# Optimization experiments

Measured on AMD Instinct MI355X. Metric: run time of the kernel, lower is better.

Reference implementation:

```python
import jax, jax.numpy as jnp
import numpy as np

B, N, C = 4, 4096, 64
K1, K2 = 4, 6
MLP1 = [128, 64, 64]
MLP2 = [128, 64]
EPS = 1e-5


def _sqdist(a, b):
    # a: [B,N,3], b: [B,M,3] -> [B,N,M]
    return (jnp.sum(a * a, -1)[:, :, None] + jnp.sum(b * b, -1)[:, None, :]
            - 2.0 * jnp.einsum('bnc,bmc->bnm', a, b))


def _knn_idx(k, xyz, new_xyz):
    # matches knn_point: topk of -square_distance(new_xyz, xyz)
    _, idx = jax.lax.top_k(-_sqdist(new_xyz, xyz), k)
    return idx  # [B,S,k]


def _gather(points, idx):
    # index_points: points [B,N,C], idx [B,S,K] -> [B,S,K,C]
    return jax.vmap(lambda p, i: p[i])(points, idx)


def _conv_bn_relu(x, w, g, b):
    # 1x1 Conv2d (no bias) + BatchNorm2d (train mode) + ReLU, channels-last
    y = jnp.einsum('bnkc,oc->bnko', x, w)
    m = jnp.mean(y, axis=(0, 1, 2), keepdims=True)
    v = jnp.var(y, axis=(0, 1, 2), keepdims=True)
    return jax.nn.relu((y - m) * jax.lax.rsqrt(v + EPS) * g + b)


def _quat_mul(a, b):
    # Hamilton product, matches mul_q_point ordering
    aw, ax, ay, az = a[..., 0], a[..., 1], a[..., 2], a[..., 3]
    bw, bx, by, bz = b[..., 0], b[..., 1], b[..., 2], b[..., 3]
    return jnp.stack([
        aw * bw - ax * bx - ay * by - az * bz,
        aw * bx + ax * bw + ay * bz - az * by,
        aw * by - ax * bz + ay * bw + az * bx,
        aw * bz + ax * by - ay * bx + az * bw], axis=-1)


def _inv_q(q):
    n2 = jnp.sum(q * q, -1, keepdims=True) + 1e-10
    return jnp.concatenate([q[..., :1], -q[..., 1:]], -1) / n2


def _qrot(q, v):
    # rotate points v [B,M,3] by quaternion q [B,4] via q * (0,v) * q^-1
    vq = jnp.concatenate([jnp.zeros(v.shape[:-1] + (1,), v.dtype), v], -1)
    qb = q[:, None, :]
    return _quat_mul(_quat_mul(qb, vq), _inv_q(q)[:, None, :])[..., 1:]


def setup_inputs() -> dict:
    key = jax.random.key(0)
    ks = jax.random.split(key, 32)

    def rn(i, shape, s=1.0):
        return jax.random.normal(ks[i], shape, jnp.float32) * s

    inp = {
        'pos1': rn(0, (B, N, 3)),
        'pos2': rn(1, (B, N, 3)),
        'feat1': rn(2, (B, N, C)),
        'feat2': rn(3, (B, N, C)),
        'q_coarse': rn(4, (B, 4)),
        't_coarse': rn(5, (B, 3)),
    }
    c1 = [2 * C + 3] + MLP1
    for i in range(len(MLP1)):
        inp['w1_%d' % i] = rn(6 + i, (c1[i + 1], c1[i]), 0.1)
        inp['g1_%d' % i] = jnp.ones((c1[i + 1],), jnp.float32)
        inp['b1_%d' % i] = jnp.zeros((c1[i + 1],), jnp.float32)
    c2 = [MLP1[-1] + C + 3] + MLP2
    for i in range(len(MLP2)):
        inp['w2_%d' % i] = rn(12 + i, (c2[i + 1], c2[i]), 0.1)
        inp['g2_%d' % i] = jnp.ones((c2[i + 1],), jnp.float32)
        inp['b2_%d' % i] = jnp.zeros((c2[i + 1],), jnp.float32)
    inp['wq'] = rn(20, (4, MLP2[-1]), 0.01)
    inp['bq'] = jnp.zeros((4,), jnp.float32)
    inp['wt'] = rn(21, (3, MLP2[-1]), 0.01)
    inp['bt'] = jnp.zeros((3,), jnp.float32)
    return inp


def reference(pos1, pos2, feat1, feat2, q_coarse, t_coarse,
              w1_0, g1_0, b1_0, w1_1, g1_1, b1_1, w1_2, g1_2, b1_2,
              w2_0, g2_0, b2_0, w2_1, g2_1, b2_1, wq, bq, wt, bt):
    # warp pos1 by the coarse pose (q, t)
    pos1_w = _qrot(q_coarse, pos1) + t_coarse[:, None, :]

    # cross-cloud KNN grouping (FlowEmbedding first stage)
    idx2 = _knn_idx(K2, pos2, pos1_w)                      # [B,N,K2]
    xd2 = _gather(pos2, idx2) - pos1_w[:, :, None, :]      # [B,N,K2,3]
    f2g = _gather(feat2, idx2)                             # [B,N,K2,C]
    f1r = jnp.broadcast_to(feat1[:, :, None, :], (B, N, K2, C))
    x = jnp.concatenate([xd2, f2g, f1r], -1)               # [B,N,K2,131]
    for w, g, b in ((w1_0, g1_0, b1_0), (w1_1, g1_1, b1_1), (w1_2, g1_2, b1_2)):
        x = _conv_bn_relu(x, w, g, b)
    fe = jnp.sum(x, axis=2)                                # [B,N,64] sum pool over neighbors

    # self KNN grouping (FlowEmbedding second stage)
    idx1 = _knn_idx(K1, pos1_w, pos1_w)                    # [B,N,K1]
    xd1 = _gather(pos1_w, idx1) - pos1_w[:, :, None, :]
    feg = _gather(fe, idx1)
    f1r2 = jnp.broadcast_to(feat1[:, :, None, :], (B, N, K1, C))
    x = jnp.concatenate([xd1, feg, f1r2], -1)              # [B,N,K1,131]
    for w, g, b in ((w2_0, g2_0, b2_0), (w2_1, g2_1, b2_1)):
        x = _conv_bn_relu(x, w, g, b)
    pooled = jnp.sum(jnp.sum(x, axis=2), axis=1)           # [B,64] sum pool

    # pose delta heads + quaternion composition
    q_det = pooled @ wq.T + bq
    q_det = q_det / (jnp.linalg.norm(q_det, axis=-1, keepdims=True) + 1e-10)
    t_det = pooled @ wt.T + bt
    q_new = _quat_mul(q_det, q_coarse)
    q_new = q_new / (jnp.linalg.norm(q_new, axis=-1, keepdims=True) + 1e-10)
    t_new = _qrot(q_det, t_coarse[:, None, :])[:, 0, :] + t_det
    return jnp.concatenate([q_new, t_new], -1)             # [B,7]
```

## Files before the change

### kernel.cpp

```cpp
#include <hip/hip_runtime.h>
#include <math.h>

#define B_ 4
#define N_ 4096
#define C_ 64
#define K1_ 4
#define K2_ 6
#define EPS_ 1e-5f
#define BN_ (B_ * N_)
#define NCH_ 8
#define CHP_ 512
#define STKD_ 16

typedef __attribute__((ext_vector_type(8))) short bf16x8;
typedef __attribute__((ext_vector_type(4))) float f32x4;
typedef __attribute__((ext_vector_type(2))) float f32x2;

__device__ __forceinline__ unsigned short f2bf(float f) {
  unsigned int u = __float_as_uint(f);
  unsigned int r = (u + 0x7fffu + ((u >> 16) & 1u)) >> 16;
  return (unsigned short)r;
}
__device__ __forceinline__ float bf2f(unsigned short u) {
  return __uint_as_float(((unsigned int)u) << 16);
}
__device__ __forceinline__ void unpack8(uint4 u, float* f) {
  unsigned* up = (unsigned*)&u;
#pragma unroll
  for (int w = 0; w < 4; ++w) {
    f[2 * w] = __uint_as_float(up[w] << 16);
    f[2 * w + 1] = __uint_as_float(up[w] & 0xFFFF0000u);
  }
}

template <int K>
__device__ __forceinline__ void insKi(int* kd, int k) {
  int x = k;
#pragma unroll
  for (int u = 0; u < K; ++u) {
    int lo = min(kd[u], x);
    x = max(kd[u], x);
    kd[u] = lo;
  }
}

__global__ __launch_bounds__(256) void k_init(
    const float* __restrict__ w1_0, const float* __restrict__ w1_1,
    const float* __restrict__ w1_2, const float* __restrict__ w2_0,
    const float* __restrict__ w2_1, unsigned short* __restrict__ Wf2a,
    unsigned short* __restrict__ Wf1a, unsigned short* __restrict__ Wfe,
    unsigned short* __restrict__ Wf1b, unsigned short* __restrict__ wb1,
    unsigned short* __restrict__ wb2, unsigned short* __restrict__ wb4,
    const float* __restrict__ pos1, const float* __restrict__ pos2,
    const float* __restrict__ qc, const float* __restrict__ tc,
    float4* __restrict__ pts4w, float4* __restrict__ pts4p,
    float4* __restrict__ pairW, float4* __restrict__ pairP,
    float* __restrict__ zbase) {
  int t = blockIdx.x * 256 + threadIdx.x;
  int m = blockIdx.y;
  if (m < 7) {
    switch (m) {
      case 0:
        if (t < 8192) Wf2a[t] = f2bf(w1_0[(t >> 6) * 131 + 3 + (t & 63)]);
        break;
      case 1:
        if (t < 8192) Wf1a[t] = f2bf(w1_0[(t >> 6) * 131 + 67 + (t & 63)]);
        break;
      case 2:
        if (t < 8192) Wfe[t] = f2bf(w2_0[(t >> 6) * 131 + 3 + (t & 63)]);
        break;
      case 3:
        if (t < 8192) Wf1b[t] = f2bf(w2_0[(t >> 6) * 131 + 67 + (t & 63)]);
        break;
      case 4:
        if (t < 8192) wb1[t] = f2bf(w1_1[t]);
        break;
      case 5:
        if (t < 4096) wb2[t] = f2bf(w1_2[t]);
        break;
      default:
        if (t < 8192) wb4[t] = f2bf(w2_1[t]);
        break;
    }
    return;
  }
  if (m == 8) {
    if (t < 10240) zbase[t] = 0.f;
    return;
  }
  if (t >= BN_) return;
  int b = t / N_;
  float qw = qc[b * 4 + 0], qx = qc[b * 4 + 1], qy = qc[b * 4 + 2], qz = qc[b * 4 + 3];
  float vx = pos1[t * 3 + 0], vy = pos1[t * 3 + 1], vz = pos1[t * 3 + 2];
  float aw = -(qx * vx + qy * vy + qz * vz);
  float ax = qw * vx + qy * vz - qz * vy;
  float ay = qw * vy - qx * vz + qz * vx;
  float az = qw * vz + qx * vy - qy * vx;
  float n2 = qw * qw + qx * qx + qy * qy + qz * qz + 1e-10f;
  float bw = qw / n2, bx = -qx / n2, by = -qy / n2, bz = -qz / n2;
  float rx = aw * bx + ax * bw + ay * bz - az * by;
  float ry = aw * by - ax * bz + ay * bw + az * bx;
  float rz = aw * bz + ax * by - ay * bx + az * bw;
  rx += tc[b * 3 + 0];
  ry += tc[b * 3 + 1];
  rz += tc[b * 3 + 2];
  float rw2 = rx * rx + ry * ry + rz * rz;
  pts4w[t] = make_float4(rx, ry, rz, rw2);
  int p = t >> 1, h = t & 1;
  float* bwp = (float*)&pairW[(size_t)2 * p];
  bwp[0 + h] = rx; bwp[2 + h] = ry; bwp[4 + h] = rz; bwp[6 + h] = rw2;
  float px = pos2[t * 3 + 0], py = pos2[t * 3 + 1], pz = pos2[t * 3 + 2];
  float pw2 = px * px + py * py + pz * pz;
  pts4p[t] = make_float4(px, py, pz, pw2);
  float* bpp = (float*)&pairP[(size_t)2 * p];
  bpp[0 + h] = px; bpp[2 + h] = py; bpp[4 + h] = pz; bpp[6 + h] = pw2;
}

__device__ __forceinline__ void proj_mfma_tail(const unsigned short* Xs, int tid,
                                               int row0,
                                               const unsigned short* __restrict__ Wb,
                                               unsigned short* __restrict__ dst) {
  constexpr int SP = 72;
  int l = tid & 63, wv = tid >> 6;
  int lm = l & 15, quad = l >> 4;
  int n0 = wv * 32;
  f32x4 acc[4][2];
#pragma unroll
  for (int rt = 0; rt < 4; ++rt)
#pragma unroll
    for (int ct = 0; ct < 2; ++ct) acc[rt][ct] = (f32x4)(0.f);
#pragma unroll
  for (int k0 = 0; k0 < 64; k0 += 32) {
    bf16x8 a[4], b[2];
#pragma unroll
    for (int rt = 0; rt < 4; ++rt)
      a[rt] = *(const bf16x8*)&Xs[(rt * 16 + lm) * SP + k0 + quad * 8];
#pragma unroll
    for (int ct = 0; ct < 2; ++ct)
      b[ct] = *(const bf16x8*)&Wb[(size_t)(n0 + ct * 16 + lm) * 64 + k0 + quad * 8];
#pragma unroll
    for (int rt = 0; rt < 4; ++rt)
#pragma unroll
      for (int ct = 0; ct < 2; ++ct)
        acc[rt][ct] =
            __builtin_amdgcn_mfma_f32_16x16x32_bf16(a[rt], b[ct], acc[rt][ct], 0, 0, 0);
  }
#pragma unroll
  for (int rt = 0; rt < 4; ++rt)
#pragma unroll
    for (int ct = 0; ct < 2; ++ct)
#pragma unroll
      for (int r = 0; r < 4; ++r) {
        int row = row0 + rt * 16 + quad * 4 + r;
        dst[(size_t)row * 128 + n0 + ct * 16 + lm] = f2bf(acc[rt][ct][r]);
      }
}

template <int K>
__device__ __forceinline__ void knn_chunk(const f32x4* __restrict__ PT, int base,
                                          float4 qv, int tid, int (*st)[256],
                                          int* __restrict__ orow) {
  f32x2 qq2 = (f32x2)(qv.w);
  f32x2 m2x = (f32x2)(-2.f * qv.x);
  f32x2 m2y = (f32x2)(-2.f * qv.y);
  f32x2 m2z = (f32x2)(-2.f * qv.z);
  int kd[K];
#pragma unroll
  for (int t = 0; t < K; ++t) kd[t] = 0x7fffffff;
  int kbd = 0x7fffffff;
  int ptr = 0;
  for (int jj = 0; jj < CHP_; jj += 8) {
    f32x2 d[4];
#pragma unroll
    for (int gq = 0; gq < 2; ++gq) {
      f32x4 e0 = PT[jj + gq * 4 + 0];
      f32x4 e1 = PT[jj + gq * 4 + 1];
      f32x4 e2 = PT[jj + gq * 4 + 2];
      f32x4 e3 = PT[jj + gq * 4 + 3];
      d[gq * 2 + 0] = __builtin_elementwise_fma(
          m2x, e0.xy,
          __builtin_elementwise_fma(m2y, e0.zw,
                                    __builtin_elementwise_fma(m2z, e1.xy, e1.zw + qq2)));
      d[gq * 2 + 1] = __builtin_elementwise_fma(
          m2x, e2.xy,
          __builtin_elementwise_fma(m2y, e2.zw,
                                    __builtin_elementwise_fma(m2z, e3.xy, e3.zw + qq2)));
    }
    int j0 = base + jj;
#pragma unroll
    for (int p = 0; p < 4; ++p) {
      int ka = (int)((__float_as_uint(d[p].x) & 0xFFFFF000u) | (unsigned)(j0 + 2 * p));
      int kb = (int)((__float_as_uint(d[p].y) & 0xFFFFF000u) | (unsigned)(j0 + 2 * p + 1));
      st[ptr][tid] = ka;
      ptr += (ka < kbd) ? 1 : 0;
      st[ptr][tid] = kb;
      ptr += (kb < kbd) ? 1 : 0;
    }
    if (__ballot(ptr >= STKD_ - 8)) {
      for (int i = 0; i < ptr; ++i) insKi<K>(kd, st[i][tid]);
      ptr = 0;
      kbd = kd[K - 1];
    }
  }
  for (int i = 0; i < ptr; ++i) insKi<K>(kd, st[i][tid]);
#pragma unroll
  for (int t = 0; t < K; ++t) orow[t] = kd[t];
}

__global__ __launch_bounds__(256) void k_knnproj(
    const float4* __restrict__ pts4w, const float4* __restrict__ pairW,
    const float4* __restrict__ pairP, int* __restrict__ outK,
    const float* __restrict__ feat2, const unsigned short* __restrict__ Wf2a,
    unsigned short* __restrict__ P2a, const float* __restrict__ feat1,
    const unsigned short* __restrict__ Wf1a, unsigned short* __restrict__ P1a,
    const unsigned short* __restrict__ Wf1b, unsigned short* __restrict__ P1b) {
  __shared__ int st[STKD_][256];
  int tid = threadIdx.x;
  int bid = blockIdx.x;
  if (bid < 768) {
    const float* src;
    const unsigned short* Wb;
    unsigned short* dst;
    switch (bid >> 8) {
      case 0: src = feat2; Wb = Wf2a; dst = P2a; break;
      case 1: src = feat1; Wb = Wf1a; dst = P1a; break;
      default: src = feat1; Wb = Wf1b; dst = P1b; break;
    }
    unsigned short* Xs = (unsigned short*)&st[0][0];
    int row0 = (bid & 255) * 64;
    for (int e = tid; e < 64 * 16; e += 256) {
      int r = e >> 4, s = e & 15;
      float4 v = *(const float4*)&src[(size_t)(row0 + r) * 64 + s * 4];
      ushort4 o;
      o.x = f2bf(v.x); o.y = f2bf(v.y); o.z = f2bf(v.z); o.w = f2bf(v.w);
      *(ushort4*)&Xs[r * 72 + s * 4] = o;
    }
    __syncthreads();
    proj_mfma_tail(Xs, tid, row0, Wb, dst);
    return;
  }
  int kbid = bid - 768;
  int x = kbid & 15, y = (kbid >> 4) & 7, z = kbid >> 7;
  int b = z & 3;
  int which = z >> 2;
  const f32x4* __restrict__ PT =
      (const f32x4*)((which ? pairW : pairP) + (size_t)b * N_ + y * CHP_);
  int base = y * CHP_;
  int n = x * 256 + tid;
  float4 qv = pts4w[(size_t)b * N_ + n];
  int* orow = &outK[((size_t)which * BN_ * NCH_ + (size_t)(b * N_ + n) * NCH_ + y) * 6];
  if (which == 0)
    knn_chunk<6>(PT, base, qv, tid, st, orow);
  else
    knn_chunk<4>(PT, base, qv, tid, st, orow);
}

__global__ __launch_bounds__(256) void k_feproj(const unsigned short* __restrict__ y3,
                                                const float* __restrict__ stat,
                                                const float* __restrict__ g,
                                                const float* __restrict__ bb,
                                                const unsigned short* __restrict__ Wfe,
                                                unsigned short* __restrict__ Pfe) {
  constexpr int SP = 72;
  __shared__ unsigned short Xs[64 * SP];
  __shared__ float scl[C_], shf[C_];
  int tid = threadIdx.x;
  if (tid < C_) {
    int c = tid;
    float s = 0.f, s2 = 0.f;
#pragma unroll
    for (int u = 0; u < 8; ++u) {
      s += stat[c * 8 + u];
      s2 += stat[C_ * 8 + c * 8 + u];
    }
    const float invM = 1.f / (float)(BN_ * K2_);
    float m = s * invM;
    float v = s2 * invM - m * m;
    float sc = g[c] * rsqrtf(v + EPS_);
    scl[c] = sc;
    shf[c] = bb[c] - m * sc;
  }
  __syncthreads();
  int row0 = blockIdx.x * 64;
  for (int e = tid; e < 64 * 16; e += 256) {
    int r = e >> 4, s = e & 15;
    size_t base = ((size_t)(row0 + r) * K2_) * C_ + s * 4;
    float a0 = 0.f, a1 = 0.f, a2 = 0.f, a3 = 0.f;
#pragma unroll
    for (int k = 0; k < K2_; ++k) {
      ushort4 u = *(const ushort4*)&y3[base + (size_t)k * C_];
      a0 += fmaxf(fmaf(bf2f(u.x), scl[s * 4 + 0], shf[s * 4 + 0]), 0.f);
      a1 += fmaxf(fmaf(bf2f(u.y), scl[s * 4 + 1], shf[s * 4 + 1]), 0.f);
      a2 += fmaxf(fmaf(bf2f(u.z), scl[s * 4 + 2], shf[s * 4 + 2]), 0.f);
      a3 += fmaxf(fmaf(bf2f(u.w), scl[s * 4 + 3], shf[s * 4 + 3]), 0.f);
    }
    ushort4 o;
    o.x = f2bf(a0); o.y = f2bf(a1); o.z = f2bf(a2); o.w = f2bf(a3);
    *(ushort4*)&Xs[r * SP + s * 4] = o;
  }
  __syncthreads();
  proj_mfma_tail(Xs, tid, row0, Wfe, Pfe);
}

template <int KNN>
__global__ __launch_bounds__(256) void k_asm(
    const float* __restrict__ Wfull,
    const float4* __restrict__ nbrPts, const float4* __restrict__ qryPts,
    const unsigned short* __restrict__ Pj, const unsigned short* __restrict__ Pn,
    const int* __restrict__ outK,
    unsigned short* __restrict__ yout, float* __restrict__ statOut) {
  __shared__ float Wx[3][128];
  __shared__ float red[16][128];
  __shared__ int idxL[33][6];
  int tid = threadIdx.x;
  int row0 = blockIdx.x * 128;
  int first = row0 / KNN;
  int nq = (row0 + 127) / KNN - first + 1;
  if (tid < 128) {
    Wx[0][tid] = Wfull[tid * 131 + 0];
    Wx[1][tid] = Wfull[tid * 131 + 1];
    Wx[2][tid] = Wfull[tid * 131 + 2];
  }
  if (tid < nq) {
    int q = first + tid;
    int km[6];
#pragma unroll
    for (int u = 0; u < 6; ++u) km[u] = 0x7fffffff;
    size_t ib = (size_t)q * (NCH_ * 6);
    if (KNN == 6) {
      for (int c = 0; c < NCH_ * 6; ++c) insKi<6>(km, outK[ib + c]);
    } else {
      for (int ch = 0; ch < NCH_; ++ch)
#pragma unroll
        for (int u = 0; u < 4; ++u) insKi<4>(km, outK[ib + ch * 6 + u]);
    }
#pragma unroll
    for (int u = 0; u < KNN; ++u) idxL[tid][u] = km[u] & 0xFFF;
  }
  __syncthreads();
  int cg = tid & 15, rg = tid >> 4;
  int c0 = cg * 8;
  float wx0[8], wx1[8], wx2[8];
#pragma unroll
  for (int u = 0; u < 8; ++u) {
    wx0[u] = Wx[0][c0 + u];
    wx1[u] = Wx[1][c0 + u];
    wx2[u] = Wx[2][c0 + u];
  }
  float s1[8], s2[8];
#pragma unroll
  for (int u = 0; u < 8; ++u) { s1[u] = 0.f; s2[u] = 0.f; }
#pragma unroll
  for (int i = 0; i < 8; ++i) {
    int row = row0 + rg * 8 + i;
    int g = row / KNN;
    int j = idxL[g - first][row - g * KNN];
    int gj = ((g >> 12) << 12) + j;
    float4 pw = qryPts[g];
    float4 pn4 = nbrPts[gj];
    float xd0 = pn4.x - pw.x;
    float xd1 = pn4.y - pw.y;
    float xd2 = pn4.z - pw.z;
    uint4 uj = *(const uint4*)&Pj[(size_t)gj * 128 + c0];
    uint4 un = *(const uint4*)&Pn[(size_t)g * 128 + c0];
    float yj[8], yn[8];
    unpack8(uj, yj);
    unpack8(un, yn);
    ushort4 o0, o1;
    unsigned short ob[8];
#pragma unroll
    for (int u = 0; u < 8; ++u) {
      float v = yj[u] + yn[u];
      v = fmaf(xd0, wx0[u], v);
      v = fmaf(xd1, wx1[u], v);
      v = fmaf(xd2, wx2[u], v);
      s1[u] += v;
      s2[u] = fmaf(v, v, s2[u]);
      ob[u] = f2bf(v);
    }
    o0.x = ob[0]; o0.y = ob[1]; o0.z = ob[2]; o0.w = ob[3];
    o1.x = ob[4]; o1.y = ob[5]; o1.z = ob[6]; o1.w = ob[7];
    *(ushort4*)&yout[(size_t)row * 128 + c0] = o0;
    *(ushort4*)&yout[(size_t)row * 128 + c0 + 4] = o1;
  }
  int slot = blockIdx.x & 7;
#pragma unroll
  for (int u = 0; u < 8; ++u) red[rg][c0 + u] = s1[u];
  __syncthreads();
  if (tid < 128) {
    float s = 0.f;
#pragma unroll
    for (int r = 0; r < 16; ++r) s += red[r][tid];
    atomicAdd(&statOut[tid * 8 + slot], s);
  }
  __syncthreads();
#pragma unroll
  for (int u = 0; u < 8; ++u) red[rg][c0 + u] = s2[u];
  __syncthreads();
  if (tid < 128) {
    float s = 0.f;
#pragma unroll
    for (int r = 0; r < 16; ++r) s += red[r][tid];
    atomicAdd(&statOut[128 * 8 + tid * 8 + slot], s);
  }
}

template <int CIN, int COUT, int KP>
__global__ __launch_bounds__(256) void k_layer_mfma(
    const unsigned short* __restrict__ Wb,
    const unsigned short* __restrict__ yprev,
    const float* __restrict__ statPrev, const float* __restrict__ gPrev,
    const float* __restrict__ bPrev, float prevInvM,
    unsigned short* __restrict__ yout,
    float* __restrict__ statOut) {
  constexpr int SP = KP + 8;
  constexpr int CST = COUT + 8;
  constexpr int CT = COUT / 64;
  __shared__ unsigned short Xs[64 * SP];
  __shared__ float scl[CIN];
  __shared__ float shf[CIN];

  int tid = threadIdx.x;
  int row0 = blockIdx.x * 64;

  for (int c = tid; c < CIN; c += 256) {
    float s = 0.f, s2 = 0.f;
#pragma unroll
    for (int u = 0; u < 8; ++u) {
      s += statPrev[c * 8 + u];
      s2 += statPrev[CIN * 8 + c * 8 + u];
    }
    float m = s * prevInvM;
    float v = s2 * prevInvM - m * m;
    float sc = gPrev[c] * rsqrtf(v + EPS_);
    scl[c] = sc;
    shf[c] = bPrev[c] - m * sc;
  }
  __syncthreads();
  constexpr int S8 = KP / 8;
  for (int e = tid; e < 64 * S8; e += 256) {
    int r = e / S8, s = e - r * S8;
    int row = row0 + r;
    uint4 u = *(const uint4*)&yprev[(size_t)row * CIN + s * 8];
    uint4 o;
    unsigned* up = (unsigned*)&u;
    unsigned* op = (unsigned*)&o;
#pragma unroll
    for (int w = 0; w < 4; ++w) {
      int c = s * 8 + w * 2;
      float lo = __uint_as_float(up[w] << 16);
      float hi = __uint_as_float(up[w] & 0xFFFF0000u);
      float rl = fmaxf(fmaf(lo, scl[c], shf[c]), 0.f);
      float rh = fmaxf(fmaf(hi, scl[c + 1], shf[c + 1]), 0.f);
      op[w] = (unsigned)f2bf(rl) | ((unsigned)f2bf(rh) << 16);
    }
    *(uint4*)&Xs[r * SP + s * 8] = o;
  }
  __syncthreads();

  int l = tid & 63, wv = tid >> 6;
  int lm = l & 15, quad = l >> 4;
  int n0 = wv * (COUT / 4);

  f32x4 acc[4][CT];
#pragma unroll
  for (int rt = 0; rt < 4; ++rt)
#pragma unroll
    for (int ct = 0; ct < CT; ++ct) acc[rt][ct] = (f32x4)(0.f);

#pragma unroll
  for (int k0 = 0; k0 < KP; k0 += 32) {
    bf16x8 a[4], b[CT];
#pragma unroll
    for (int rt = 0; rt < 4; ++rt)
      a[rt] = *(const bf16x8*)&Xs[(rt * 16 + lm) * SP + k0 + quad * 8];
#pragma unroll
    for (int ct = 0; ct < CT; ++ct)
      b[ct] = *(const bf16x8*)&Wb[(size_t)(n0 + ct * 16 + lm) * KP + k0 + quad * 8];
#pragma unroll
    for (int rt = 0; rt < 4; ++rt)
#pragma unroll
      for (int ct = 0; ct < CT; ++ct)
        acc[rt][ct] =
            __builtin_amdgcn_mfma_f32_16x16x32_bf16(a[rt], b[ct], acc[rt][ct], 0, 0, 0);
  }

  int slot = blockIdx.x & 7;
#pragma unroll
  for (int ct = 0; ct < CT; ++ct) {
    float s1 = 0.f, s2 = 0.f;
#pragma unroll
    for (int rt = 0; rt < 4; ++rt)
#pragma unroll
      for (int r = 0; r < 4; ++r) {
        float v = acc[rt][ct][r];
        s1 += v;
        s2 += v * v;
      }
    s1 += __shfl_xor(s1, 16);
    s1 += __shfl_xor(s1, 32);
    s2 += __shfl_xor(s2, 16);
    s2 += __shfl_xor(s2, 32);
    if (quad == 0) {
      int col = n0 + ct * 16 + lm;
      atomicAdd(&statOut[col * 8 + slot], s1);
      atomicAdd(&statOut[COUT * 8 + col * 8 + slot], s2);
    }
  }

  __syncthreads();
  unsigned short* Ys = Xs;
#pragma unroll
  for (int rt = 0; rt < 4; ++rt)
#pragma unroll
    for (int ct = 0; ct < CT; ++ct)
#pragma unroll
      for (int r = 0; r < 4; ++r)
        Ys[(rt * 16 + quad * 4 + r) * CST + n0 + ct * 16 + lm] = f2bf(acc[rt][ct][r]);
  __syncthreads();
  constexpr int SO = COUT / 8;
  for (int e = tid; e < 64 * SO; e += 256) {
    int r = e / SO, c0 = (e - r * SO) * 8;
    uint4 v = *(const uint4*)&Ys[r * CST + c0];
    *(uint4*)&yout[((size_t)(row0 + r)) * COUT + c0] = v;
  }
}

__global__ __launch_bounds__(256) void k_pooled(const unsigned short* __restrict__ y5,
                                                const float* __restrict__ stat,
                                                const float* __restrict__ g,
                                                const float* __restrict__ bb,
                                                float* __restrict__ pooled) {
  __shared__ float scl[C_], shf[C_];
  __shared__ float red[16][C_];
  if (threadIdx.x < C_) {
    int c = threadIdx.x;
    float s = 0.f, s2 = 0.f;
#pragma unroll
    for (int u = 0; u < 8; ++u) {
      s += stat[c * 8 + u];
      s2 += stat[C_ * 8 + c * 8 + u];
    }
    const float invM = 1.f / (float)(BN_ * K1_);
    float m = s * invM;
    float v = s2 * invM - m * m;
    float sc = g[c] * rsqrtf(v + EPS_);
    scl[c] = sc;
    shf[c] = bb[c] - m * sc;
  }
  __syncthreads();
  int cq = threadIdx.x & 15, rr = threadIdx.x >> 4;
  int c0 = cq * 4;
  int row0 = blockIdx.x * 64;
  int b = blockIdx.x >> 8;
  float a0 = 0.f, a1 = 0.f, a2 = 0.f, a3 = 0.f;
#pragma unroll
  for (int i = 0; i < 4; ++i) {
    int row = row0 + rr * 4 + i;
    ushort4 u = *(const ushort4*)&y5[(size_t)row * C_ + c0];
    a0 += fmaxf(fmaf(bf2f(u.x), scl[c0 + 0], shf[c0 + 0]), 0.f);
    a1 += fmaxf(fmaf(bf2f(u.y), scl[c0 + 1], shf[c0 + 1]), 0.f);
    a2 += fmaxf(fmaf(bf2f(u.z), scl[c0 + 2], shf[c0 + 2]), 0.f);
    a3 += fmaxf(fmaf(bf2f(u.w), scl[c0 + 3], shf[c0 + 3]), 0.f);
  }
  red[rr][c0 + 0] = a0;
  red[rr][c0 + 1] = a1;
  red[rr][c0 + 2] = a2;
  red[rr][c0 + 3] = a3;
  __syncthreads();
  if (threadIdx.x < C_) {
    float s = 0.f;
#pragma unroll
    for (int r = 0; r < 16; ++r) s += red[r][threadIdx.x];
    atomicAdd(&pooled[(b * C_ + threadIdx.x) * 8 + (blockIdx.x & 7)], s);
  }
}

__global__ void k_final(const float* __restrict__ pooled, const float* __restrict__ wq,
                        const float* __restrict__ bq, const float* __restrict__ wt,
                        const float* __restrict__ bt, const float* __restrict__ qc,
                        const float* __restrict__ tc, float* __restrict__ out) {
  int b = threadIdx.x;
  if (b >= B_) return;
  float P[C_];
#pragma unroll
  for (int c = 0; c < C_; ++c) {
    float s = 0.f;
#pragma unroll
    for (int u = 0; u < 8; ++u) s += pooled[(b * C_ + c) * 8 + u];
    P[c] = s;
  }
  float qd[4];
#pragma unroll
  for (int i = 0; i < 4; ++i) {
    float s = bq[i];
#pragma unroll
    for (int c = 0; c < C_; ++c) s = fmaf(P[c], wq[i * C_ + c], s);
    qd[i] = s;
  }
  float td[3];
#pragma unroll
  for (int i = 0; i < 3; ++i) {
    float s = bt[i];
#pragma unroll
    for (int c = 0; c < C_; ++c) s = fmaf(P[c], wt[i * C_ + c], s);
    td[i] = s;
  }
  float nq = sqrtf(qd[0] * qd[0] + qd[1] * qd[1] + qd[2] * qd[2] + qd[3] * qd[3]) + 1e-10f;
#pragma unroll
  for (int i = 0; i < 4; ++i) qd[i] /= nq;
  float cw = qc[b * 4 + 0], cx = qc[b * 4 + 1], cyy = qc[b * 4 + 2], cz = qc[b * 4 + 3];
  float qnw = qd[0] * cw - qd[1] * cx - qd[2] * cyy - qd[3] * cz;
  float qnx = qd[0] * cx + qd[1] * cw + qd[2] * cz - qd[3] * cyy;
  float qny = qd[0] * cyy - qd[1] * cz + qd[2] * cw + qd[3] * cx;
  float qnz = qd[0] * cz + qd[1] * cyy - qd[2] * cx + qd[3] * cw;
  float nn = sqrtf(qnw * qnw + qnx * qnx + qny * qny + qnz * qnz) + 1e-10f;
  float vx = tc[b * 3 + 0], vy = tc[b * 3 + 1], vz = tc[b * 3 + 2];
  float aw = -(qd[1] * vx + qd[2] * vy + qd[3] * vz);
  float ax = qd[0] * vx + qd[2] * vz - qd[3] * vy;
  float ay = qd[0] * vy - qd[1] * vz + qd[3] * vx;
  float az = qd[0] * vz + qd[1] * vy - qd[2] * vx;
  float n2 = qd[0] * qd[0] + qd[1] * qd[1] + qd[2] * qd[2] + qd[3] * qd[3] + 1e-10f;
  float bw = qd[0] / n2, bx = -qd[1] / n2, by = -qd[2] / n2, bz = -qd[3] / n2;
  float rx = aw * bx + ax * bw + ay * bz - az * by;
  float ry = aw * by - ax * bz + ay * bw + az * bx;
  float rz = aw * bz + ax * by - ay * bx + az * bw;
  out[b * 7 + 0] = qnw / nn;
  out[b * 7 + 1] = qnx / nn;
  out[b * 7 + 2] = qny / nn;
  out[b * 7 + 3] = qnz / nn;
  out[b * 7 + 4] = rx + td[0];
  out[b * 7 + 5] = ry + td[1];
  out[b * 7 + 6] = rz + td[2];
}

extern "C" void kernel_launch(void* const* d_in, const int* in_sizes, int n_in,
                              void* d_out, int out_size, void* d_ws, size_t ws_size,
                              hipStream_t stream) {
  const float* pos1 = (const float*)d_in[0];
  const float* pos2 = (const float*)d_in[1];
  const float* feat1 = (const float*)d_in[2];
  const float* feat2 = (const float*)d_in[3];
  const float* qc = (const float*)d_in[4];
  const float* tc = (const float*)d_in[5];
  const float* w1_0 = (const float*)d_in[6];
  const float* g1_0 = (const float*)d_in[7];
  const float* b1_0 = (const float*)d_in[8];
  const float* w1_1 = (const float*)d_in[9];
  const float* g1_1 = (const float*)d_in[10];
  const float* b1_1 = (const float*)d_in[11];
  const float* w1_2 = (const float*)d_in[12];
  const float* g1_2 = (const float*)d_in[13];
  const float* b1_2 = (const float*)d_in[14];
  const float* w2_0 = (const float*)d_in[15];
  const float* g2_0 = (const float*)d_in[16];
  const float* b2_0 = (const float*)d_in[17];
  const float* w2_1 = (const float*)d_in[18];
  const float* g2_1 = (const float*)d_in[19];
  const float* b2_1 = (const float*)d_in[20];
  const float* wq = (const float*)d_in[21];
  const float* bq = (const float*)d_in[22];
  const float* wt = (const float*)d_in[23];
  const float* bt = (const float*)d_in[24];

  float* ws = (float*)d_ws;
  const size_t off_stat = 0;
  const size_t off_pool = 8192;
  const size_t off_wb = 10240;
  const size_t off_pts4w = 36864;
  const size_t off_pts4p = 102400;
  const size_t off_pairW = 167936;
  const size_t off_pairP = 233472;
  const size_t off_knnK = 299008;
  const size_t off_P2a = 1871872;
  const size_t off_P1a = 2920448;
  const size_t off_P1b = 3969024;
  const size_t off_Pfe = 5017600;
  const size_t off_yA = 6066176;
  const size_t off_yB = 12357632;

  float* stat0 = ws + off_stat;
  float* stat1 = stat0 + 2048;
  float* stat2 = stat1 + 1024;
  float* stat3 = stat2 + 1024;
  float* stat4 = stat3 + 2048;
  float* pooled = ws + off_pool;
  unsigned short* Wf2a = (unsigned short*)(ws + off_wb);
  unsigned short* Wf1a = Wf2a + 8192;
  unsigned short* Wfe = Wf1a + 8192;
  unsigned short* Wf1b = Wfe + 8192;
  unsigned short* wb1 = Wf1b + 8192;
  unsigned short* wb2 = wb1 + 8192;
  unsigned short* wb4 = wb2 + 4096;
  float4* pts4w = (float4*)(ws + off_pts4w);
  float4* pts4p = (float4*)(ws + off_pts4p);
  float4* pairW = (float4*)(ws + off_pairW);
  float4* pairP = (float4*)(ws + off_pairP);
  int* knnK = (int*)(ws + off_knnK);
  unsigned short* P2a = (unsigned short*)(ws + off_P2a);
  unsigned short* P1a = (unsigned short*)(ws + off_P1a);
  unsigned short* P1b = (unsigned short*)(ws + off_P1b);
  unsigned short* Pfe = (unsigned short*)(ws + off_Pfe);
  unsigned short* yA = (unsigned short*)(ws + off_yA);
  unsigned short* yB = (unsigned short*)(ws + off_yB);

  k_init<<<dim3(64, 9), 256, 0, stream>>>(w1_0, w1_1, w1_2, w2_0, w2_1, Wf2a, Wf1a,
                                          Wfe, Wf1b, wb1, wb2, wb4, pos1, pos2, qc, tc,
                                          pts4w, pts4p, pairW, pairP, ws + off_stat);

  k_knnproj<<<dim3(768 + 1024), 256, 0, stream>>>(pts4w, pairW, pairP, knnK, feat2,
                                                  Wf2a, P2a, feat1, Wf1a, P1a, Wf1b,
                                                  P1b);

  k_asm<K2_><<<dim3(98304 / 128), 256, 0, stream>>>(w1_0, pts4p, pts4w, P2a, P1a, knnK,
                                                    yA, stat0);
  k_layer_mfma<128, 64, 128><<<dim3(1536), 256, 0, stream>>>(
      wb1, yA, stat0, g1_0, b1_0, 1.f / 98304.f, yB, stat1);
  k_layer_mfma<64, 64, 64><<<dim3(1536), 256, 0, stream>>>(
      wb2, yB, stat1, g1_1, b1_1, 1.f / 98304.f, yA, stat2);
  k_feproj<<<dim3(256), 256, 0, stream>>>(yA, stat2, g1_2, b1_2, Wfe, Pfe);
  k_asm<K1_><<<dim3(65536 / 128), 256, 0, stream>>>(
      w2_0, pts4w, pts4w, Pfe, P1b, knnK + (size_t)BN_ * NCH_ * 6, yA, stat3);
  k_layer_mfma<128, 64, 128><<<dim3(1024), 256, 0, stream>>>(
      wb4, yA, stat3, g2_0, b2_0, 1.f / 65536.f, yB, stat4);
  k_pooled<<<dim3(65536 / 64), 256, 0, stream>>>(yB, stat4, g2_1, b2_1, pooled);
  k_final<<<dim3(1), 64, 0, stream>>>(pooled, wq, bq, wt, bt, qc, tc, (float*)d_out);
}
```

Measured before the change: 358.8 us.

## Recompute gathered first-layer activations instead of materializing 128-channel intermediate

The assembly kernel now only computes batch-norm statistics and writes the resolved neighbor indices, no longer storing the 128-channel bf16 pre-activation tensor. The next layer kernel re-gathers the projected features and positions by index, recomputes the pre-activation, applies BN+ReLU and feeds the MFMA directly. This removes a large write and read of the intermediate tensor at the cost of doing the gather and arithmetic twice. The layer kernels are also specialised to a fixed 64-column output.

```diff
diff --git a/kernel.cpp b/kernel.cpp
--- a/kernel.cpp
+++ b/kernel.cpp
@@ -303,12 +303,11 @@
 }
 
 template <int KNN>
-__global__ __launch_bounds__(256) void k_asm(
-    const float* __restrict__ Wfull,
-    const float4* __restrict__ nbrPts, const float4* __restrict__ qryPts,
-    const unsigned short* __restrict__ Pj, const unsigned short* __restrict__ Pn,
-    const int* __restrict__ outK,
-    unsigned short* __restrict__ yout, float* __restrict__ statOut) {
+__global__ __launch_bounds__(256) void k_stat0(
+    const float* __restrict__ Wfull, const float4* __restrict__ nbrPts,
+    const float4* __restrict__ qryPts, const unsigned short* __restrict__ Pj,
+    const unsigned short* __restrict__ Pn, const int* __restrict__ outK,
+    int* __restrict__ idxM, float* __restrict__ statOut) {
   __shared__ float Wx[3][128];
   __shared__ float red[16][128];
   __shared__ int idxL[33][6];
@@ -334,8 +333,13 @@
 #pragma unroll
         for (int u = 0; u < 4; ++u) insKi<4>(km, outK[ib + ch * 6 + u]);
     }
-#pragma unroll
-    for (int u = 0; u < KNN; ++u) idxL[tid][u] = km[u] & 0xFFF;
+    int bb = (q >> 12) << 12;
+#pragma unroll
+    for (int u = 0; u < KNN; ++u) {
+      int gj = bb + (km[u] & 0xFFF);
+      idxL[tid][u] = gj;
+      idxM[(size_t)q * KNN + u] = gj;
+    }
   }
   __syncthreads();
   int cg = tid & 15, rg = tid >> 4;
@@ -354,8 +358,7 @@
   for (int i = 0; i < 8; ++i) {
     int row = row0 + rg * 8 + i;
     int g = row / KNN;
-    int j = idxL[g - first][row - g * KNN];
-    int gj = ((g >> 12) << 12) + j;
+    int gj = idxL[g - first][row - g * KNN];
     float4 pw = qryPts[g];
     float4 pn4 = nbrPts[gj];
     float xd0 = pn4.x - pw.x;
@@ -366,8 +369,6 @@
     float yj[8], yn[8];
     unpack8(uj, yj);
     unpack8(un, yn);
-    ushort4 o0, o1;
-    unsigned short ob[8];
 #pragma unroll
     for (int u = 0; u < 8; ++u) {
       float v = yj[u] + yn[u];
@@ -376,12 +377,7 @@
       v = fmaf(xd2, wx2[u], v);
       s1[u] += v;
       s2[u] = fmaf(v, v, s2[u]);
-      ob[u] = f2bf(v);
-    }
-    o0.x = ob[0]; o0.y = ob[1]; o0.z = ob[2]; o0.w = ob[3];
-    o1.x = ob[4]; o1.y = ob[5]; o1.z = ob[6]; o1.w = ob[7];
-    *(ushort4*)&yout[(size_t)row * 128 + c0] = o0;
-    *(ushort4*)&yout[(size_t)row * 128 + c0 + 4] = o1;
+    }
   }
   int slot = blockIdx.x & 7;
 #pragma unroll
@@ -405,30 +401,35 @@
   }
 }
 
-template <int CIN, int COUT, int KP>
-__global__ __launch_bounds__(256) void k_layer_mfma(
+template <int KNN>
+__global__ __launch_bounds__(256) void k_layerG(
     const unsigned short* __restrict__ Wb,
-    const unsigned short* __restrict__ yprev,
+    const float* __restrict__ Wfull, const float4* __restrict__ nbrPts,
+    const float4* __restrict__ qryPts, const unsigned short* __restrict__ Pj,
+    const unsigned short* __restrict__ Pn, const int* __restrict__ idxM,
     const float* __restrict__ statPrev, const float* __restrict__ gPrev,
     const float* __restrict__ bPrev, float prevInvM,
     unsigned short* __restrict__ yout,
     float* __restrict__ statOut) {
+  constexpr int KP = 128, COUT = 64;
   constexpr int SP = KP + 8;
   constexpr int CST = COUT + 8;
-  constexpr int CT = COUT / 64;
   __shared__ unsigned short Xs[64 * SP];
-  __shared__ float scl[CIN];
-  __shared__ float shf[CIN];
+  __shared__ float scl[KP];
+  __shared__ float shf[KP];
+  __shared__ float Wx[3][128];
+  __shared__ int gjL[64];
+  __shared__ float xdL[3][64];
 
   int tid = threadIdx.x;
   int row0 = blockIdx.x * 64;
 
-  for (int c = tid; c < CIN; c += 256) {
+  for (int c = tid; c < KP; c += 256) {
     float s = 0.f, s2 = 0.f;
 #pragma unroll
     for (int u = 0; u < 8; ++u) {
       s += statPrev[c * 8 + u];
-      s2 += statPrev[CIN * 8 + c * 8 + u];
+      s2 += statPrev[KP * 8 + c * 8 + u];
     }
     float m = s * prevInvM;
     float v = s2 * prevInvM - m * m;
@@ -436,64 +437,78 @@
     scl[c] = sc;
     shf[c] = bPrev[c] - m * sc;
   }
-  __syncthreads();
-  constexpr int S8 = KP / 8;
-  for (int e = tid; e < 64 * S8; e += 256) {
-    int r = e / S8, s = e - r * S8;
+  if (tid < 128) {
+    Wx[0][tid] = Wfull[tid * 131 + 0];
+    Wx[1][tid] = Wfull[tid * 131 + 1];
+    Wx[2][tid] = Wfull[tid * 131 + 2];
+  }
+  if (tid < 64) {
+    int row = row0 + tid;
+    int g = row / KNN;
+    int gj = idxM[(size_t)g * KNN + (row - g * KNN)];
+    gjL[tid] = gj;
+    float4 pw = qryPts[g];
+    float4 pn4 = nbrPts[gj];
+    xdL[0][tid] = pn4.x - pw.x;
+    xdL[1][tid] = pn4.y - pw.y;
+    xdL[2][tid] = pn4.z - pw.z;
+  }
+  __syncthreads();
+  for (int e = tid; e < 64 * 16; e += 256) {
+    int r = e >> 4, s = e & 15;
+    int c0 = s * 8;
     int row = row0 + r;
-    uint4 u = *(const uint4*)&yprev[(size_t)row * CIN + s * 8];
-    uint4 o;
-    unsigned* up = (unsigned*)&u;
-    unsigned* op = (unsigned*)&o;
-#pragma unroll
-    for (int w = 0; w < 4; ++w) {
-      int c = s * 8 + w * 2;
-      float lo = __uint_as_float(up[w] << 16);
-      float hi = __uint_as_float(up[w] & 0xFFFF0000u);
-      float rl = fmaxf(fmaf(lo, scl[c], shf[c]), 0.f);
-      float rh = fmaxf(fmaf(hi, scl[c + 1], shf[c + 1]), 0.f);
-      op[w] = (unsigned)f2bf(rl) | ((unsigned)f2bf(rh) << 16);
-    }
-    *(uint4*)&Xs[r * SP + s * 8] = o;
+    int g = row / KNN;
+    uint4 uj = *(const uint4*)&Pj[(size_t)gjL[r] * 128 + c0];
+    uint4 un = *(const uint4*)&Pn[(size_t)g * 128 + c0];
+    float yj[8], yn[8];
+    unpack8(uj, yj);
+    unpack8(un, yn);
+    float xd0 = xdL[0][r], xd1 = xdL[1][r], xd2 = xdL[2][r];
+    unsigned short ob[8];
+#pragma unroll
+    for (int u = 0; u < 8; ++u) {
+      int c = c0 + u;
+      float v = yj[u] + yn[u];
+      v = fmaf(xd0, Wx[0][c], v);
+      v = fmaf(xd1, Wx[1][c], v);
+      v = fmaf(xd2, Wx[2][c], v);
+      ob[u] = f2bf(fmaxf(fmaf(v, scl[c], shf[c]), 0.f));
+    }
+    ushort4 o0, o1;
+    o0.x = ob[0]; o0.y = ob[1]; o0.z = ob[2]; o0.w = ob[3];
+    o1.x = ob[4]; o1.y = ob[5]; o1.z = ob[6]; o1.w = ob[7];
+    *(ushort4*)&Xs[r * SP + c0] = o0;
+    *(ushort4*)&Xs[r * SP + c0 + 4] = o1;
   }
   __syncthreads();
 
   int l = tid & 63, wv = tid >> 6;
   int lm = l & 15, quad = l >> 4;
-  int n0 = wv * (COUT / 4);
-
-  f32x4 acc[4][CT];
-#pragma unroll
-  for (int rt = 0; rt < 4; ++rt)
-#pragma unroll
-    for (int ct = 0; ct < CT; ++ct) acc[rt][ct] = (f32x4)(0.f);
+  int n0 = wv * 16;
+
+  f32x4 acc[4];
+#pragma unroll
+  for (int rt = 0; rt < 4; ++rt) acc[rt] = (f32x4)(0.f);
 
 #pragma unroll
   for (int k0 = 0; k0 < KP; k0 += 32) {
-    bf16x8 a[4], b[CT];
+    bf16x8 b = *(const bf16x8*)&Wb[(size_t)(n0 + lm) * KP + k0 + quad * 8];
+#pragma unroll
+    for (int rt = 0; rt < 4; ++rt) {
+      bf16x8 a = *(const bf16x8*)&Xs[(rt * 16 + lm) * SP + k0 + quad * 8];
+      acc[rt] = __builtin_amdgcn_mfma_f32_16x16x32_bf16(a, b, acc[rt], 0, 0, 0);
+    }
+  }
+
+  int slot = blockIdx.x & 7;
+  {
+    float s1 = 0.f, s2 = 0.f;
 #pragma unroll
     for (int rt = 0; rt < 4; ++rt)
-      a[rt] = *(const bf16x8*)&Xs[(rt * 16 + lm) * SP + k0 + quad * 8];
-#pragma unroll
-    for (int ct = 0; ct < CT; ++ct)
-      b[ct] = *(const bf16x8*)&Wb[(size_t)(n0 + ct * 16 + lm) * KP + k0 + quad * 8];
-#pragma unroll
-    for (int rt = 0; rt < 4; ++rt)
-#pragma unroll
-      for (int ct = 0; ct < CT; ++ct)
-        acc[rt][ct] =
-            __builtin_amdgcn_mfma_f32_16x16x32_bf16(a[rt], b[ct], acc[rt][ct], 0, 0, 0);
-  }
-
-  int slot = blockIdx.x & 7;
-#pragma unroll
-  for (int ct = 0; ct < CT; ++ct) {
-    float s1 = 0.f, s2 = 0.f;
-#pragma unroll
-    for (int rt = 0; rt < 4; ++rt)
 #pragma unroll
       for (int r = 0; r < 4; ++r) {
-        float v = acc[rt][ct][r];
+        float v = acc[rt][r];
         s1 += v;
         s2 += v * v;
       }
@@ -502,7 +517,7 @@
     s2 += __shfl_xor(s2, 16);
     s2 += __shfl_xor(s2, 32);
     if (quad == 0) {
-      int col = n0 + ct * 16 + lm;
+      int col = n0 + lm;
       atomicAdd(&statOut[col * 8 + slot], s1);
       atomicAdd(&statOut[COUT * 8 + col * 8 + slot], s2);
     }
@@ -513,14 +528,115 @@
 #pragma unroll
   for (int rt = 0; rt < 4; ++rt)
 #pragma unroll
-    for (int ct = 0; ct < CT; ++ct)
-#pragma unroll
-      for (int r = 0; r < 4; ++r)
-        Ys[(rt * 16 + quad * 4 + r) * CST + n0 + ct * 16 + lm] = f2bf(acc[rt][ct][r]);
-  __syncthreads();
-  constexpr int SO = COUT / 8;
-  for (int e = tid; e < 64 * SO; e += 256) {
-    int r = e / SO, c0 = (e - r * SO) * 8;
+    for (int r = 0; r < 4; ++r)
+      Ys[(rt * 16 + quad * 4 + r) * CST + n0 + lm] = f2bf(acc[rt][r]);
+  __syncthreads();
+  for (int e = tid; e < 64 * 8; e += 256) {
+    int r = e >> 3, c0 = (e & 7) * 8;
+    uint4 v = *(const uint4*)&Ys[r * CST + c0];
+    *(uint4*)&yout[((size_t)(row0 + r)) * COUT + c0] = v;
+  }
+}
+
+__global__ __launch_bounds__(256) void k_layer64(
+    const unsigned short* __restrict__ Wb,
+    const unsigned short* __restrict__ yprev,
+    const float* __restrict__ statPrev, const float* __restrict__ gPrev,
+    const float* __restrict__ bPrev, float prevInvM,
+    unsigned short* __restrict__ yout, float* __restrict__ statOut) {
+  constexpr int KP = 64, COUT = 64;
+  constexpr int SP = KP + 8;
+  constexpr int CST = COUT + 8;
+  __shared__ unsigned short Xs[64 * SP];
+  __shared__ float scl[KP];
+  __shared__ float shf[KP];
+
+  int tid = threadIdx.x;
+  int row0 = blockIdx.x * 64;
+
+  for (int c = tid; c < KP; c += 256) {
+    float s = 0.f, s2 = 0.f;
+#pragma unroll
+    for (int u = 0; u < 8; ++u) {
+      s += statPrev[c * 8 + u];
+      s2 += statPrev[KP * 8 + c * 8 + u];
+    }
+    float m = s * prevInvM;
+    float v = s2 * prevInvM - m * m;
+    float sc = gPrev[c] * rsqrtf(v + EPS_);
+    scl[c] = sc;
+    shf[c] = bPrev[c] - m * sc;
+  }
+  __syncthreads();
+  for (int e = tid; e < 64 * 8; e += 256) {
+    int r = e >> 3, s = e & 7;
+    int row = row0 + r;
+    uint4 u = *(const uint4*)&yprev[(size_t)row * KP + s * 8];
+    uint4 o;
+    unsigned* up = (unsigned*)&u;
+    unsigned* op = (unsigned*)&o;
+#pragma unroll
+    for (int w = 0; w < 4; ++w) {
+      int c = s * 8 + w * 2;
+      float lo = __uint_as_float(up[w] << 16);
+      float hi = __uint_as_float(up[w] & 0xFFFF0000u);
+      float rl = fmaxf(fmaf(lo, scl[c], shf[c]), 0.f);
+      float rh = fmaxf(fmaf(hi, scl[c + 1], shf[c + 1]), 0.f);
+      op[w] = (unsigned)f2bf(rl) | ((unsigned)f2bf(rh) << 16);
+    }
+    *(uint4*)&Xs[r * SP + s * 8] = o;
+  }
+  __syncthreads();
+
+  int l = tid & 63, wv = tid >> 6;
+  int lm = l & 15, quad = l >> 4;
+  int n0 = wv * 16;
+
+  f32x4 acc[4];
+#pragma unroll
+  for (int rt = 0; rt < 4; ++rt) acc[rt] = (f32x4)(0.f);
+#pragma unroll
+  for (int k0 = 0; k0 < KP; k0 += 32) {
+    bf16x8 b = *(const bf16x8*)&Wb[(size_t)(n0 + lm) * KP + k0 + quad * 8];
+#pragma unroll
+    for (int rt = 0; rt < 4; ++rt) {
+      bf16x8 a = *(const bf16x8*)&Xs[(rt * 16 + lm) * SP + k0 + quad * 8];
+      acc[rt] = __builtin_amdgcn_mfma_f32_16x16x32_bf16(a, b, acc[rt], 0, 0, 0);
+    }
+  }
+
+  int slot = blockIdx.x & 7;
+  {
+    float s1 = 0.f, s2 = 0.f;
+#pragma unroll
+    for (int rt = 0; rt < 4; ++rt)
+#pragma unroll
+      for (int r = 0; r < 4; ++r) {
+        float v = acc[rt][r];
+        s1 += v;
+        s2 += v * v;
+      }
+    s1 += __shfl_xor(s1, 16);
+    s1 += __shfl_xor(s1, 32);
+    s2 += __shfl_xor(s2, 16);
+    s2 += __shfl_xor(s2, 32);
+    if (quad == 0) {
+      int col = n0 + lm;
+      atomicAdd(&statOut[col * 8 + slot], s1);
+      atomicAdd(&statOut[COUT * 8 + col * 8 + slot], s2);
+    }
+  }
+
+  __syncthreads();
+  unsigned short* Ys = Xs;
+#pragma unroll
+  for (int rt = 0; rt < 4; ++rt)
+#pragma unroll
+    for (int r = 0; r < 4; ++r)
+      Ys[(rt * 16 + quad * 4 + r) * CST + n0 + lm] = f2bf(acc[rt][r]);
+  __syncthreads();
+  for (int e = tid; e < 64 * 8; e += 256) {
+    int r = e >> 3, c0 = (e & 7) * 8;
     uint4 v = *(const uint4*)&Ys[r * CST + c0];
     *(uint4*)&yout[((size_t)(row0 + r)) * COUT + c0] = v;
   }
@@ -672,12 +788,14 @@
   const size_t off_pairW = 167936;
   const size_t off_pairP = 233472;
   const size_t off_knnK = 299008;
-  const size_t off_P2a = 1871872;
-  const size_t off_P1a = 2920448;
-  const size_t off_P1b = 3969024;
-  const size_t off_Pfe = 5017600;
-  const size_t off_yA = 6066176;
-  const size_t off_yB = 12357632;
+  const size_t off_idxM1 = 1871872;
+  const size_t off_idxM2 = 1970176;
+  const size_t off_P2a = 2035712;
+  const size_t off_P1a = 3084288;
+  const size_t off_P1b = 4132864;
+  const size_t off_Pfe = 5181440;
+  const size_t off_yA = 6230016;
+  const size_t off_yB = 9375744;
 
   float* stat0 = ws + off_stat;
   float* stat1 = stat0 + 2048;
@@ -697,6 +815,8 @@
   float4* pairW = (float4*)(ws + off_pairW);
   float4* pairP = (float4*)(ws + off_pairP);
   int* knnK = (int*)(ws + off_knnK);
+  int* idxM1 = (int*)(ws + off_idxM1);
+  int* idxM2 = (int*)(ws + off_idxM2);
   unsigned short* P2a = (unsigned short*)(ws + off_P2a);
   unsigned short* P1a = (unsigned short*)(ws + off_P1a);
   unsigned short* P1b = (unsigned short*)(ws + off_P1b);
@@ -712,17 +832,19 @@
                                                   Wf2a, P2a, feat1, Wf1a, P1a, Wf1b,
                                                   P1b);
 
-  k_asm<K2_><<<dim3(98304 / 128), 256, 0, stream>>>(w1_0, pts4p, pts4w, P2a, P1a, knnK,
-                                                    yA, stat0);
-  k_layer_mfma<128, 64, 128><<<dim3(1536), 256, 0, stream>>>(
-      wb1, yA, stat0, g1_0, b1_0, 1.f / 98304.f, yB, stat1);
-  k_layer_mfma<64, 64, 64><<<dim3(1536), 256, 0, stream>>>(
-      wb2, yB, stat1, g1_1, b1_1, 1.f / 98304.f, yA, stat2);
-  k_feproj<<<dim3(256), 256, 0, stream>>>(yA, stat2, g1_2, b1_2, Wfe, Pfe);
-  k_asm<K1_><<<dim3(65536 / 128), 256, 0, stream>>>(
-      w2_0, pts4w, pts4w, Pfe, P1b, knnK + (size_t)BN_ * NCH_ * 6, yA, stat3);
-  k_layer_mfma<128, 64, 128><<<dim3(1024), 256, 0, stream>>>(
-      wb4, yA, stat3, g2_0, b2_0, 1.f / 65536.f, yB, stat4);
-  k_pooled<<<dim3(65536 / 64), 256, 0, stream>>>(yB, stat4, g2_1, b2_1, pooled);
+  k_stat0<K2_><<<dim3(98304 / 128), 256, 0, stream>>>(w1_0, pts4p, pts4w, P2a, P1a,
+                                                      knnK, idxM1, stat0);
+  k_layerG<K2_><<<dim3(98304 / 64), 256, 0, stream>>>(
+      wb1, w1_0, pts4p, pts4w, P2a, P1a, idxM1, stat0, g1_0, b1_0, 1.f / 98304.f, yA,
+      stat1);
+  k_layer64<<<dim3(98304 / 64), 256, 0, stream>>>(wb2, yA, stat1, g1_1, b1_1,
+                                                  1.f / 98304.f, yB, stat2);
+  k_feproj<<<dim3(256), 256, 0, stream>>>(yB, stat2, g1_2, b1_2, Wfe, Pfe);
+  k_stat0<K1_><<<dim3(65536 / 128), 256, 0, stream>>>(
+      w2_0, pts4w, pts4w, Pfe, P1b, knnK + (size_t)BN_ * NCH_ * 6, idxM2, stat3);
+  k_layerG<K1_><<<dim3(65536 / 64), 256, 0, stream>>>(
+      wb4, w2_0, pts4w, pts4w, Pfe, P1b, idxM2, stat3, g2_0, b2_0, 1.f / 65536.f, yA,
+      stat4);
+  k_pooled<<<dim3(65536 / 64), 256, 0, stream>>>(yA, stat4, g2_1, b2_1, pooled);
   k_final<<<dim3(1), 64, 0, stream>>>(pooled, wq, bq, wt, bt, qc, tc, (float*)d_out);
 }
```

New measurement: 357.2 us (median of 2 runs). About the same (-0.5%).
